# Performance work log

Measured on AMD Instinct MI355X. Metric: run time of the kernel, lower is better.

Reference implementation:

```python
import jax, jax.numpy as jnp
import numpy as np

MAX_DEPTH = 10
NUM_INPUT = 256
NUM_OUTPUT = 64
BATCH = 131072
N_INTERNAL = 2**MAX_DEPTH - 1  # 1023 heap-indexed internal nodes
N_LEAVES = 2**MAX_DEPTH        # 1024 leaves


def setup_inputs() -> dict:
    key = jax.random.key(0)
    k_x, k_w, k_b, k_a, k_l = jax.random.split(key, 5)
    x = jax.random.normal(k_x, (BATCH, NUM_INPUT), dtype=jnp.float32)
    # internal-node params (torch init: weights ~ N(0,0.1); bias/alpha zeros,
    # but we randomize bias/alpha so both branches are exercised)
    W = jax.random.normal(k_w, (N_INTERNAL, NUM_INPUT), dtype=jnp.float32) * 0.1
    b = jax.random.normal(k_b, (N_INTERNAL,), dtype=jnp.float32) * 0.1
    alpha = jax.random.normal(k_a, (N_INTERNAL,), dtype=jnp.float32)
    leaves = jax.random.normal(k_l, (N_LEAVES, NUM_OUTPUT), dtype=jnp.float32)
    return {"x": x, "W": W, "b": b, "alpha": alpha, "leaves": leaves}


def reference(x, W, b, alpha, leaves):
    # Batched hard root-to-leaf traversal of the soft binary tree.
    # Heap indexing: node i -> left child 2i+1, right child 2i+2.
    B = x.shape[0]
    idx = jnp.zeros((B,), dtype=jnp.int32)
    mult = jnp.ones((B,), dtype=x.dtype)
    for _ in range(MAX_DEPTH):  # fixed small structural loop over depth levels
        w = W[idx]  # [B, F] gather of per-node weights
        val = jax.nn.sigmoid(alpha[idx] * (jnp.einsum('bf,bf->b', x, w) + b[idx]))
        go_right = val >= 0.5
        # right branch contributes val, left branch contributes (1 - val)
        mult = mult * jnp.where(go_right, val, 1.0 - val)
        idx = 2 * idx + 1 + go_right.astype(jnp.int32)
    leaf_idx = idx - N_INTERNAL  # [B]
    return mult[:, None] * leaves[leaf_idx]  # [B, num_output]
```

## Files before the change

kernel.cpp:

```cpp
#include <hip/hip_runtime.h>

#define NUM_INPUT   256
#define NUM_OUTPUT  64
#define N_INTERNAL  1023
#define STAGED_NODES 31
#define THREADS 512
#define NBLOCKS 1024

__device__ __forceinline__ float group16_reduce_add(float acc) {
    int t;
    t = __builtin_amdgcn_update_dpp(0, __float_as_int(acc), 0x121, 0xf, 0xf, true);
    acc += __int_as_float(t);
    t = __builtin_amdgcn_update_dpp(0, __float_as_int(acc), 0x122, 0xf, 0xf, true);
    acc += __int_as_float(t);
    t = __builtin_amdgcn_update_dpp(0, __float_as_int(acc), 0x124, 0xf, 0xf, true);
    acc += __int_as_float(t);
    t = __builtin_amdgcn_update_dpp(0, __float_as_int(acc), 0x128, 0xf, 0xf, true);
    acc += __int_as_float(t);
    return acc;
}

__device__ __forceinline__ float group16_reduce_mul(float v) {
    int t;
    t = __builtin_amdgcn_update_dpp(0, __float_as_int(v), 0x121, 0xf, 0xf, true);
    v *= __int_as_float(t);
    t = __builtin_amdgcn_update_dpp(0, __float_as_int(v), 0x122, 0xf, 0xf, true);
    v *= __int_as_float(t);
    t = __builtin_amdgcn_update_dpp(0, __float_as_int(v), 0x124, 0xf, 0xf, true);
    v *= __int_as_float(t);
    t = __builtin_amdgcn_update_dpp(0, __float_as_int(v), 0x128, 0xf, 0xf, true);
    v *= __int_as_float(t);
    return v;
}

#define XISSUE(E, X0, X1, X2, X3)                                           \
    {                                                                       \
        const float4* xp_ = reinterpret_cast<const float4*>(                \
            x + (size_t)(gbase + 4 * (E)) * NUM_INPUT);                     \
        X0 = xp_[s]; X1 = xp_[16 + s]; X2 = xp_[32 + s]; X3 = xp_[48 + s];  \
        __builtin_amdgcn_sched_barrier(0);                                  \
    }

#define LSTEP(IDX, ZND, X0, X1, X2, X3)                                     \
    {                                                                       \
        float a_i = lds_a[IDX];                                             \
        float b_i = lds_b[IDX];                                             \
        const float4* wr_ = reinterpret_cast<const float4*>(                \
            lds_w + (size_t)(IDX) * NUM_INPUT);                             \
        float4 w0 = wr_[s], w1 = wr_[16 + s], w2 = wr_[32 + s], w3 = wr_[48 + s]; \
        float a0 = X0.x * w0.x, a1 = X1.x * w1.x;                           \
        float a2 = X2.x * w2.x, a3 = X3.x * w3.x;                           \
        a0 = fmaf(X0.y, w0.y, a0); a1 = fmaf(X1.y, w1.y, a1);               \
        a2 = fmaf(X2.y, w2.y, a2); a3 = fmaf(X3.y, w3.y, a3);               \
        a0 = fmaf(X0.z, w0.z, a0); a1 = fmaf(X1.z, w1.z, a1);               \
        a2 = fmaf(X2.z, w2.z, a2); a3 = fmaf(X3.z, w3.z, a3);               \
        a0 = fmaf(X0.w, w0.w, a0); a1 = fmaf(X1.w, w1.w, a1);               \
        a2 = fmaf(X2.w, w2.w, a2); a3 = fmaf(X3.w, w3.w, a3);               \
        float acc_ = group16_reduce_add((a0 + a1) + (a2 + a3));             \
        float z = a_i * (acc_ + b_i);                                       \
        ZND = __int_as_float(__float_as_int(z) | 0x80000000);               \
        IDX = 2 * (IDX) + 1 + ((z >= 0.0f) ? 1 : 0);                        \
    }

#define DISSUE(IDX)                                                         \
    {                                                                       \
        const float4* wr_ = reinterpret_cast<const float4*>(                \
            W + (size_t)(IDX) * NUM_INPUT);                                 \
        wd0 = wr_[s]; wd1 = wr_[16 + s]; wd2 = wr_[32 + s]; wd3 = wr_[48 + s]; \
    }
#define DCONSUME(IDX, ZND, X0, X1, X2, X3)                                  \
    {                                                                       \
        float a_i = lds_a[IDX];                                             \
        float b_i = lds_b[IDX];                                             \
        float a0 = X0.x * wd0.x, a1 = X1.x * wd1.x;                         \
        float a2 = X2.x * wd2.x, a3 = X3.x * wd3.x;                         \
        a0 = fmaf(X0.y, wd0.y, a0); a1 = fmaf(X1.y, wd1.y, a1);             \
        a2 = fmaf(X2.y, wd2.y, a2); a3 = fmaf(X3.y, wd3.y, a3);             \
        a0 = fmaf(X0.z, wd0.z, a0); a1 = fmaf(X1.z, wd1.z, a1);             \
        a2 = fmaf(X2.z, wd2.z, a2); a3 = fmaf(X3.z, wd3.z, a3);             \
        a0 = fmaf(X0.w, wd0.w, a0); a1 = fmaf(X1.w, wd1.w, a1);             \
        a2 = fmaf(X2.w, wd2.w, a2); a3 = fmaf(X3.w, wd3.w, a3);             \
        float acc_ = group16_reduce_add((a0 + a1) + (a2 + a3));             \
        float z = a_i * (acc_ + b_i);                                       \
        ZND = __int_as_float(__float_as_int(z) | 0x80000000);               \
        IDX = 2 * (IDX) + 1 + ((z >= 0.0f) ? 1 : 0);                        \
    }

#define DL_TICK(IDXD, IDXL, ZD5, ZD6, ZD7, ZD8, ZD9, ZL0, ZL1, ZL2, ZL3, ZL4, \
                XD0, XD1, XD2, XD3, XL0, XL1, XL2, XL3)                     \
    DISSUE(IDXD)                                                            \
    LSTEP(IDXL, ZL0, XL0, XL1, XL2, XL3)                                    \
    DCONSUME(IDXD, ZD5, XD0, XD1, XD2, XD3)                                 \
    DISSUE(IDXD)                                                            \
    LSTEP(IDXL, ZL1, XL0, XL1, XL2, XL3)                                    \
    DCONSUME(IDXD, ZD6, XD0, XD1, XD2, XD3)                                 \
    DISSUE(IDXD)                                                            \
    LSTEP(IDXL, ZL2, XL0, XL1, XL2, XL3)                                    \
    DCONSUME(IDXD, ZD7, XD0, XD1, XD2, XD3)                                 \
    DISSUE(IDXD)                                                            \
    LSTEP(IDXL, ZL3, XL0, XL1, XL2, XL3)                                    \
    DCONSUME(IDXD, ZD8, XD0, XD1, XD2, XD3)                                 \
    DISSUE(IDXD)                                                            \
    LSTEP(IDXL, ZL4, XL0, XL1, XL2, XL3)                                    \
    DCONSUME(IDXD, ZD9, XD0, XD1, XD2, XD3)

#define EPI(E, IDX, Z0, Z1, Z2, Z3, Z4, Z5, Z6, Z7, Z8, Z9)                 \
    {                                                                       \
        float zsel = -1e30f;                                                \
        zsel = (s == 0) ? Z0 : zsel; zsel = (s == 1) ? Z1 : zsel;           \
        zsel = (s == 2) ? Z2 : zsel; zsel = (s == 3) ? Z3 : zsel;           \
        zsel = (s == 4) ? Z4 : zsel; zsel = (s == 5) ? Z5 : zsel;           \
        zsel = (s == 6) ? Z6 : zsel; zsel = (s == 7) ? Z7 : zsel;           \
        zsel = (s == 8) ? Z8 : zsel; zsel = (s == 9) ? Z9 : zsel;           \
        float f = 1.0f + __expf(zsel);                                      \
        float p = group16_reduce_mul(f);                                    \
        float mult = 1.0f / p;                                              \
        const int leaf = (IDX) - N_INTERNAL;                                \
        const float4 lv = reinterpret_cast<const float4*>(                  \
            leaves + (size_t)leaf * NUM_OUTPUT)[s];                         \
        float4 o;                                                           \
        o.x = mult * lv.x; o.y = mult * lv.y;                               \
        o.z = mult * lv.z; o.w = mult * lv.w;                               \
        reinterpret_cast<float4*>(                                          \
            out + (size_t)(gbase + 4 * (E)) * NUM_OUTPUT)[s] = o;           \
    }

__global__ __launch_bounds__(THREADS, 4) void ogtree_kernel(
    const float* __restrict__ x,
    const float* __restrict__ W,
    const float* __restrict__ b,
    const float* __restrict__ alpha,
    const float* __restrict__ leaves,
    float* __restrict__ out)
{
    __shared__ float lds_w[STAGED_NODES * NUM_INPUT];
    __shared__ float lds_b[N_INTERNAL];
    __shared__ float lds_a[N_INTERNAL];

    const int tid  = threadIdx.x;
    const int lane = tid & 63;
    const int wid  = tid >> 6;
    const int g    = lane >> 4;
    const int s    = lane & 15;
    const int gbase = blockIdx.x * (THREADS / 64) * 16 + wid * 16 + g;

    float4 xa0, xa1, xa2, xa3;
    float4 xb0, xb1, xb2, xb3;
    float4 xc0, xc1, xc2, xc3;

    XISSUE(0, xa0, xa1, xa2, xa3)

    {
        const float4* Wv = reinterpret_cast<const float4*>(W);
        float4* lw4 = reinterpret_cast<float4*>(lds_w);
        #pragma unroll
        for (int i = tid; i < STAGED_NODES * NUM_INPUT / 4; i += THREADS)
            lw4[i] = Wv[i];
        for (int i = tid; i < N_INTERNAL; i += THREADS) {
            lds_b[i] = b[i];
            lds_a[i] = alpha[i];
        }
    }
    __syncthreads();

    float ZA0, ZA1, ZA2, ZA3, ZA4, ZA5, ZA6, ZA7, ZA8, ZA9;
    float ZB0, ZB1, ZB2, ZB3, ZB4, ZB5, ZB6, ZB7, ZB8, ZB9;
    float4 wd0, wd1, wd2, wd3;
    int idxA, idxB;

    XISSUE(1, xb0, xb1, xb2, xb3)
    idxA = 0;
    LSTEP(idxA, ZA0, xa0, xa1, xa2, xa3)
    LSTEP(idxA, ZA1, xa0, xa1, xa2, xa3)
    LSTEP(idxA, ZA2, xa0, xa1, xa2, xa3)
    LSTEP(idxA, ZA3, xa0, xa1, xa2, xa3)
    LSTEP(idxA, ZA4, xa0, xa1, xa2, xa3)

    XISSUE(2, xc0, xc1, xc2, xc3)
    idxB = 0;
    DL_TICK(idxA, idxB, ZA5, ZA6, ZA7, ZA8, ZA9, ZB0, ZB1, ZB2, ZB3, ZB4,
            xa0, xa1, xa2, xa3, xb0, xb1, xb2, xb3)
    EPI(0, idxA, ZA0, ZA1, ZA2, ZA3, ZA4, ZA5, ZA6, ZA7, ZA8, ZA9)

    XISSUE(3, xa0, xa1, xa2, xa3)
    idxA = 0;
    DL_TICK(idxB, idxA, ZB5, ZB6, ZB7, ZB8, ZB9, ZA0, ZA1, ZA2, ZA3, ZA4,
            xb0, xb1, xb2, xb3, xc0, xc1, xc2, xc3)
    EPI(1, idxB, ZB0, ZB1, ZB2, ZB3, ZB4, ZB5, ZB6, ZB7, ZB8, ZB9)

    idxB = 0;
    DL_TICK(idxA, idxB, ZA5, ZA6, ZA7, ZA8, ZA9, ZB0, ZB1, ZB2, ZB3, ZB4,
            xc0, xc1, xc2, xc3, xa0, xa1, xa2, xa3)
    EPI(2, idxA, ZA0, ZA1, ZA2, ZA3, ZA4, ZA5, ZA6, ZA7, ZA8, ZA9)

    DISSUE(idxB)
    DCONSUME(idxB, ZB5, xa0, xa1, xa2, xa3)
    DISSUE(idxB)
    DCONSUME(idxB, ZB6, xa0, xa1, xa2, xa3)
    DISSUE(idxB)
    DCONSUME(idxB, ZB7, xa0, xa1, xa2, xa3)
    DISSUE(idxB)
    DCONSUME(idxB, ZB8, xa0, xa1, xa2, xa3)
    DISSUE(idxB)
    DCONSUME(idxB, ZB9, xa0, xa1, xa2, xa3)
    EPI(3, idxB, ZB0, ZB1, ZB2, ZB3, ZB4, ZB5, ZB6, ZB7, ZB8, ZB9)
}

extern "C" void kernel_launch(void* const* d_in, const int* in_sizes, int n_in,
                              void* d_out, int out_size, void* d_ws, size_t ws_size,
                              hipStream_t stream) {
    const float* x      = (const float*)d_in[0];
    const float* W      = (const float*)d_in[1];
    const float* b      = (const float*)d_in[2];
    const float* alpha  = (const float*)d_in[3];
    const float* leaves = (const float*)d_in[4];
    float* out = (float*)d_out;

    ogtree_kernel<<<NBLOCKS, THREADS, 0, stream>>>(x, W, b, alpha, leaves, out);
}
```

Baseline: 49.84 us.

## Interleave two rows' deep-level gathers with double-buffered weight registers

Replaces the staggered three-buffer schedule, where one row's LDS-staged shallow levels overlap another row's global-memory deep levels, with a simpler one. Each wave now handles only two row groups: both run their five shallow levels from LDS, then their deep-level global weight gathers alternate, each with its own register buffer, so one row's load is in flight while the other computes. The per-wave work is halved and the block count doubled to keep full batch coverage. This trades the cross-row overlap of LDS and global work for a shorter register live range, at the cost of staging the shared weights, bias and alpha into LDS twice as often and possibly needing a second wave of blocks.

```diff
diff --git a/kernel.cpp b/kernel.cpp
--- a/kernel.cpp
+++ b/kernel.cpp
@@ -5,7 +5,7 @@
 #define N_INTERNAL  1023
 #define STAGED_NODES 31
 #define THREADS 512
-#define NBLOCKS 1024
+#define NBLOCKS 2048
 
 __device__ __forceinline__ float group16_reduce_add(float acc) {
     int t;
@@ -62,47 +62,52 @@
         IDX = 2 * (IDX) + 1 + ((z >= 0.0f) ? 1 : 0);                        \
     }
 
-#define DISSUE(IDX)                                                         \
+#define DISSUE_A(IDX)                                                       \
     {                                                                       \
         const float4* wr_ = reinterpret_cast<const float4*>(                \
             W + (size_t)(IDX) * NUM_INPUT);                                 \
-        wd0 = wr_[s]; wd1 = wr_[16 + s]; wd2 = wr_[32 + s]; wd3 = wr_[48 + s]; \
-    }
-#define DCONSUME(IDX, ZND, X0, X1, X2, X3)                                  \
+        wa0 = wr_[s]; wa1 = wr_[16 + s]; wa2 = wr_[32 + s]; wa3 = wr_[48 + s]; \
+    }
+#define DISSUE_B(IDX)                                                       \
+    {                                                                       \
+        const float4* wr_ = reinterpret_cast<const float4*>(                \
+            W + (size_t)(IDX) * NUM_INPUT);                                 \
+        wb0 = wr_[s]; wb1 = wr_[16 + s]; wb2 = wr_[32 + s]; wb3 = wr_[48 + s]; \
+    }
+#define DCONSUME_A(IDX, ZND, X0, X1, X2, X3)                                \
     {                                                                       \
         float a_i = lds_a[IDX];                                             \
         float b_i = lds_b[IDX];                                             \
-        float a0 = X0.x * wd0.x, a1 = X1.x * wd1.x;                         \
-        float a2 = X2.x * wd2.x, a3 = X3.x * wd3.x;                         \
-        a0 = fmaf(X0.y, wd0.y, a0); a1 = fmaf(X1.y, wd1.y, a1);             \
-        a2 = fmaf(X2.y, wd2.y, a2); a3 = fmaf(X3.y, wd3.y, a3);             \
-        a0 = fmaf(X0.z, wd0.z, a0); a1 = fmaf(X1.z, wd1.z, a1);             \
-        a2 = fmaf(X2.z, wd2.z, a2); a3 = fmaf(X3.z, wd3.z, a3);             \
-        a0 = fmaf(X0.w, wd0.w, a0); a1 = fmaf(X1.w, wd1.w, a1);             \
-        a2 = fmaf(X2.w, wd2.w, a2); a3 = fmaf(X3.w, wd3.w, a3);             \
+        float a0 = X0.x * wa0.x, a1 = X1.x * wa1.x;                         \
+        float a2 = X2.x * wa2.x, a3 = X3.x * wa3.x;                         \
+        a0 = fmaf(X0.y, wa0.y, a0); a1 = fmaf(X1.y, wa1.y, a1);             \
+        a2 = fmaf(X2.y, wa2.y, a2); a3 = fmaf(X3.y, wa3.y, a3);             \
+        a0 = fmaf(X0.z, wa0.z, a0); a1 = fmaf(X1.z, wa1.z, a1);             \
+        a2 = fmaf(X2.z, wa2.z, a2); a3 = fmaf(X3.z, wa3.z, a3);             \
+        a0 = fmaf(X0.w, wa0.w, a0); a1 = fmaf(X1.w, wa1.w, a1);             \
+        a2 = fmaf(X2.w, wa2.w, a2); a3 = fmaf(X3.w, wa3.w, a3);             \
         float acc_ = group16_reduce_add((a0 + a1) + (a2 + a3));             \
         float z = a_i * (acc_ + b_i);                                       \
         ZND = __int_as_float(__float_as_int(z) | 0x80000000);               \
         IDX = 2 * (IDX) + 1 + ((z >= 0.0f) ? 1 : 0);                        \
     }
-
-#define DL_TICK(IDXD, IDXL, ZD5, ZD6, ZD7, ZD8, ZD9, ZL0, ZL1, ZL2, ZL3, ZL4, \
-                XD0, XD1, XD2, XD3, XL0, XL1, XL2, XL3)                     \
-    DISSUE(IDXD)                                                            \
-    LSTEP(IDXL, ZL0, XL0, XL1, XL2, XL3)                                    \
-    DCONSUME(IDXD, ZD5, XD0, XD1, XD2, XD3)                                 \
-    DISSUE(IDXD)                                                            \
-    LSTEP(IDXL, ZL1, XL0, XL1, XL2, XL3)                                    \
-    DCONSUME(IDXD, ZD6, XD0, XD1, XD2, XD3)                                 \
-    DISSUE(IDXD)                                                            \
-    LSTEP(IDXL, ZL2, XL0, XL1, XL2, XL3)                                    \
-    DCONSUME(IDXD, ZD7, XD0, XD1, XD2, XD3)                                 \
-    DISSUE(IDXD)                                                            \
-    LSTEP(IDXL, ZL3, XL0, XL1, XL2, XL3)                                    \
-    DCONSUME(IDXD, ZD8, XD0, XD1, XD2, XD3)                                 \
-    DISSUE(IDXD)                                                            \
-    LSTEP(IDXL, ZL4, XL0, XL1, XL2, XL3)                                    \
-    DCONSUME(IDXD, ZD9, XD0, XD1, XD2, XD3)
+#define DCONSUME_B(IDX, ZND, X0, X1, X2, X3)                                \
+    {                                                                       \
+        float a_i = lds_a[IDX];                                             \
+        float b_i = lds_b[IDX];                                             \
+        float a0 = X0.x * wb0.x, a1 = X1.x * wb1.x;                         \
+        float a2 = X2.x * wb2.x, a3 = X3.x * wb3.x;                         \
+        a0 = fmaf(X0.y, wb0.y, a0); a1 = fmaf(X1.y, wb1.y, a1);             \
+        a2 = fmaf(X2.y, wb2.y, a2); a3 = fmaf(X3.y, wb3.y, a3);             \
+        a0 = fmaf(X0.z, wb0.z, a0); a1 = fmaf(X1.z, wb1.z, a1);             \
+        a2 = fmaf(X2.z, wb2.z, a2); a3 = fmaf(X3.z, wb3.z, a3);             \
+        a0 = fmaf(X0.w, wb0.w, a0); a1 = fmaf(X1.w, wb1.w, a1);             \
+        a2 = fmaf(X2.w, wb2.w, a2); a3 = fmaf(X3.w, wb3.w, a3);             \
+        float acc_ = group16_reduce_add((a0 + a1) + (a2 + a3));             \
+        float z = a_i * (acc_ + b_i);                                       \
+        ZND = __int_as_float(__float_as_int(z) | 0x80000000);               \
+        IDX = 2 * (IDX) + 1 + ((z >= 0.0f) ? 1 : 0);                        \
+    }
 
 #define EPI(E, IDX, Z0, Z1, Z2, Z3, Z4, Z5, Z6, Z7, Z8, Z9)                 \
     {                                                                       \
@@ -142,11 +147,12 @@
     const int wid  = tid >> 6;
     const int g    = lane >> 4;
     const int s    = lane & 15;
-    const int gbase = blockIdx.x * (THREADS / 64) * 16 + wid * 16 + g;
+    const int gbase = blockIdx.x * (THREADS / 64) * 8 + wid * 8 + g;
 
     float4 xa0, xa1, xa2, xa3;
     float4 xb0, xb1, xb2, xb3;
-    float4 xc0, xc1, xc2, xc3;
+    float4 wa0, wa1, wa2, wa3;
+    float4 wb0, wb1, wb2, wb3;
 
     XISSUE(0, xa0, xa1, xa2, xa3)
 
@@ -163,47 +169,46 @@
     }
     __syncthreads();
 
+    XISSUE(1, xb0, xb1, xb2, xb3)
+
+    int idxA = 0, idxB = 0;
     float ZA0, ZA1, ZA2, ZA3, ZA4, ZA5, ZA6, ZA7, ZA8, ZA9;
     float ZB0, ZB1, ZB2, ZB3, ZB4, ZB5, ZB6, ZB7, ZB8, ZB9;
-    float4 wd0, wd1, wd2, wd3;
-    int idxA, idxB;
-
-    XISSUE(1, xb0, xb1, xb2, xb3)
-    idxA = 0;
+
     LSTEP(idxA, ZA0, xa0, xa1, xa2, xa3)
     LSTEP(idxA, ZA1, xa0, xa1, xa2, xa3)
     LSTEP(idxA, ZA2, xa0, xa1, xa2, xa3)
     LSTEP(idxA, ZA3, xa0, xa1, xa2, xa3)
     LSTEP(idxA, ZA4, xa0, xa1, xa2, xa3)
-
-    XISSUE(2, xc0, xc1, xc2, xc3)
-    idxB = 0;
-    DL_TICK(idxA, idxB, ZA5, ZA6, ZA7, ZA8, ZA9, ZB0, ZB1, ZB2, ZB3, ZB4,
-            xa0, xa1, xa2, xa3, xb0, xb1, xb2, xb3)
+    LSTEP(idxB, ZB0, xb0, xb1, xb2, xb3)
+    LSTEP(idxB, ZB1, xb0, xb1, xb2, xb3)
+    LSTEP(idxB, ZB2, xb0, xb1, xb2, xb3)
+    LSTEP(idxB, ZB3, xb0, xb1, xb2, xb3)
+    LSTEP(idxB, ZB4, xb0, xb1, xb2, xb3)
+
+    DISSUE_A(idxA)
+    DISSUE_B(idxB)
+    DCONSUME_A(idxA, ZA5, xa0, xa1, xa2, xa3)
+    DISSUE_A(idxA)
+    DCONSUME_B(idxB, ZB5, xb0, xb1, xb2, xb3)
+    DISSUE_B(idxB)
+    DCONSUME_A(idxA, ZA6, xa0, xa1, xa2, xa3)
+    DISSUE_A(idxA)
+    DCONSUME_B(idxB, ZB6, xb0, xb1, xb2, xb3)
+    DISSUE_B(idxB)
+    DCONSUME_A(idxA, ZA7, xa0, xa1, xa2, xa3)
+    DISSUE_A(idxA)
+    DCONSUME_B(idxB, ZB7, xb0, xb1, xb2, xb3)
+    DISSUE_B(idxB)
+    DCONSUME_A(idxA, ZA8, xa0, xa1, xa2, xa3)
+    DISSUE_A(idxA)
+    DCONSUME_B(idxB, ZB8, xb0, xb1, xb2, xb3)
+    DISSUE_B(idxB)
+    DCONSUME_A(idxA, ZA9, xa0, xa1, xa2, xa3)
+    DCONSUME_B(idxB, ZB9, xb0, xb1, xb2, xb3)
+
     EPI(0, idxA, ZA0, ZA1, ZA2, ZA3, ZA4, ZA5, ZA6, ZA7, ZA8, ZA9)
-
-    XISSUE(3, xa0, xa1, xa2, xa3)
-    idxA = 0;
-    DL_TICK(idxB, idxA, ZB5, ZB6, ZB7, ZB8, ZB9, ZA0, ZA1, ZA2, ZA3, ZA4,
-            xb0, xb1, xb2, xb3, xc0, xc1, xc2, xc3)
     EPI(1, idxB, ZB0, ZB1, ZB2, ZB3, ZB4, ZB5, ZB6, ZB7, ZB8, ZB9)
-
-    idxB = 0;
-    DL_TICK(idxA, idxB, ZA5, ZA6, ZA7, ZA8, ZA9, ZB0, ZB1, ZB2, ZB3, ZB4,
-            xc0, xc1, xc2, xc3, xa0, xa1, xa2, xa3)
-    EPI(2, idxA, ZA0, ZA1, ZA2, ZA3, ZA4, ZA5, ZA6, ZA7, ZA8, ZA9)
-
-    DISSUE(idxB)
-    DCONSUME(idxB, ZB5, xa0, xa1, xa2, xa3)
-    DISSUE(idxB)
-    DCONSUME(idxB, ZB6, xa0, xa1, xa2, xa3)
-    DISSUE(idxB)
-    DCONSUME(idxB, ZB7, xa0, xa1, xa2, xa3)
-    DISSUE(idxB)
-    DCONSUME(idxB, ZB8, xa0, xa1, xa2, xa3)
-    DISSUE(idxB)
-    DCONSUME(idxB, ZB9, xa0, xa1, xa2, xa3)
-    EPI(3, idxB, ZB0, ZB1, ZB2, ZB3, ZB4, ZB5, ZB6, ZB7, ZB8, ZB9)
 }
 
 extern "C" void kernel_launch(void* const* d_in, const int* in_sizes, int n_in,
```

After: 50.67 us. No clear change (+1.7%).
